# Performance work log

Measured on AMD Instinct MI355X. Metric: run time of the kernel, lower is better.

## Reference

```python
import jax, jax.numpy as jnp
import numpy as np

BS, DIM, N_CLASSES = 4096, 512, 100
POS_W, NEG_W = 2.0, 40.0
MARGIN, POS_T, NEG_T = 0.1, 0.5, 0.5


def setup_inputs() -> dict:
    key = jax.random.key(0)
    k1, k2 = jax.random.split(key)
    x = jax.random.normal(k1, (BS, DIM), dtype=jnp.float32)
    x = x / jnp.linalg.norm(x, axis=-1, keepdims=True)  # cosine-mode embeddings
    labels = jax.random.randint(k2, (BS,), 0, N_CLASSES, dtype=jnp.int64 if jax.config.jax_enable_x64 else jnp.int32)
    return {"batch": x, "labels": labels}


def _masked_logsumexp(sims, mask, use_max):
    # Faithful port of Criterion.masked_logsumexp with dim=0 (per-column).
    m = sims * mask  # bool mask promotes; masked-out entries become 0
    ref = jnp.max(m, axis=0) if use_max else jnp.min(m, axis=0)  # (BS,)
    ref = jax.lax.stop_gradient(ref)
    nz = (jnp.max(m, axis=0) + jnp.min(m, axis=0)) != 0  # columns with any nonzero masked entry
    s = jnp.sum(jnp.exp(sims - ref[None, :]) * mask, axis=0)  # (BS,)
    vals = jnp.log(jnp.where(nz, s, 1.0)) + ref
    return vals, nz


def _masked_mean_softplus(vals, nz, w):
    cnt = jnp.sum(nz).astype(vals.dtype)
    sp = jax.nn.softplus(vals) / w
    mean = jnp.sum(jnp.where(nz, sp, 0.0)) / jnp.maximum(cnt, 1.0)
    # torch path returns scalar 0 from masked_logsumexp when no nz columns -> softplus(0)/w
    return jnp.where(cnt > 0, mean, jax.nn.softplus(0.0) / w)


def reference(batch, labels):
    sim = batch @ batch.T                                  # (BS, BS) cosine similarity
    same = labels[:, None] == labels[None, :]
    diff = ~same
    eye = jnp.eye(sim.shape[0], dtype=bool)

    # per-row bounds: hardest positive (min sim, excl. self) / hardest negative (max sim)
    pos_bound = jnp.min(jnp.where(same & ~eye, sim, jnp.inf), axis=1)   # (BS,)
    neg_bound = jnp.max(jnp.where(diff, sim, -jnp.inf), axis=1)        # (BS,)

    # torch broadcasting applies bounds per-COLUMN (last dim)
    neg_mask = diff & (sim + MARGIN > pos_bound[None, :])
    pos_mask = same & (sim - MARGIN < neg_bound[None, :])

    w_pos = -POS_W * (sim - POS_T)
    w_neg = NEG_W * (sim - NEG_T)

    pos_vals, pos_nz = _masked_logsumexp(w_pos, pos_mask, use_max=False)
    neg_vals, neg_nz = _masked_logsumexp(w_neg, neg_mask, use_max=True)

    loss = _masked_mean_softplus(pos_vals, pos_nz, POS_W) \
         + _masked_mean_softplus(neg_vals, neg_nz, NEG_W)
    return loss
```

## Files before the change

kernel.cpp:

```cpp
#include <hip/hip_runtime.h>
#include <stdint.h>


#define BS 4096
#define DIM 512
#define NTILES 528
#define NSLOT 32

typedef __attribute__((ext_vector_type(8))) short short8;
typedef __attribute__((ext_vector_type(4))) float f32x4;

#define TILE_USH (128 * 64)

__device__ __forceinline__ ushort f2bf(float f){
  unsigned u = __float_as_uint(f);
  return (ushort)((u + 0x7fffu + ((u >> 16) & 1u)) >> 16);
}
__device__ __forceinline__ void gld_lds16(void* ldsp, const void* gp){
  __builtin_amdgcn_global_load_lds((const __attribute__((address_space(1))) void*)gp,
                                   (__attribute__((address_space(3))) void*)ldsp, 16, 0, 0);
}

__global__ void k_convert(const float* __restrict__ x, ushort* __restrict__ xh){
  int i = blockIdx.x * blockDim.x + threadIdx.x;
  float4 v = ((const float4*)x)[i];
  ((ushort4*)xh)[i] = make_ushort4(f2bf(v.x), f2bf(v.y), f2bf(v.z), f2bf(v.w));
}

__device__ __forceinline__ void decode_tile(int bid, int& Rm, int& Rn, bool& diag){
  int wg = (bid & 7) * 66 + (bid >> 3);
  int ii = wg, bm = 0;
  while (ii >= 32 - bm){ ii -= 32 - bm; ++bm; }
  const int bn = bm + ii;
  diag = (bm == bn);
  Rm = bm * 128; Rn = bn * 128;
}

__device__ __forceinline__ void gemm_tile(f32x4 (&acc)[4][4], ushort* lds,
                                          const ushort* __restrict__ Xh,
                                          int Rm, int Rn, int t)
{
  const int l  = t & 63;
  const int w  = t >> 6;
  const int wm = w >> 1, wn = w & 1;
  const int lc = l & 15;
  const int lq = l >> 4;
  const int r0 = t >> 3;
  const int gx = (t & 7) ^ (r0 & 7);
  const int lds_i = t * 8;

  #pragma unroll
  for (int i = 0; i < 4; ++i)
    #pragma unroll
    for (int j = 0; j < 4; ++j) acc[i][j] = (f32x4){0.f, 0.f, 0.f, 0.f};

  for (int ks = 0; ks < 8; ++ks){
    const int kb = ks * 64 + gx * 8;
    #pragma unroll
    for (int rep = 0; rep < 4; ++rep){
      const int row = rep * 32 + r0;
      const int lo  = rep * 2048 + lds_i;
      gld_lds16(&lds[lo],            Xh + (size_t)(Rm + row) * DIM + kb);
      gld_lds16(&lds[TILE_USH + lo], Xh + (size_t)(Rn + row) * DIM + kb);
    }
    __syncthreads();
    #pragma unroll
    for (int kk = 0; kk < 2; ++kk){
      const int gr = kk * 4 + lq;
      const int sl = (gr ^ (l & 7)) * 8;
      short8 ah[4], bh[4];
      #pragma unroll
      for (int f = 0; f < 4; ++f){
        ah[f] = *(const short8*)&lds[(wm * 64 + f * 16 + lc) * 64 + sl];
        bh[f] = *(const short8*)&lds[TILE_USH + (wn * 64 + f * 16 + lc) * 64 + sl];
      }
      #pragma unroll
      for (int fm = 0; fm < 4; ++fm)
        #pragma unroll
        for (int fn = 0; fn < 4; ++fn)
          acc[fm][fn] = __builtin_amdgcn_mfma_f32_16x16x32_bf16(ah[fm], bh[fn], acc[fm][fn], 0, 0, 0);
    }
    __syncthreads();
  }
}

__global__ __launch_bounds__(256)
void k_bounds(const ushort* __restrict__ Xh, const int* __restrict__ labels,
              float* __restrict__ posB, float* __restrict__ negB)
{
  __shared__ ushort lds[2 * TILE_USH];
  const int t = threadIdx.x;
  int Rm, Rn; bool diag;
  decode_tile((int)blockIdx.x, Rm, Rn, diag);
  const int bm = Rm >> 7, bn = Rn >> 7;

  f32x4 acc[4][4];
  gemm_tile(acc, lds, Xh, Rm, Rn, t);

  const int l  = t & 63;
  const int w  = t >> 6;
  const int wm = w >> 1, wn = w & 1;
  const int lc = l & 15, lq = l >> 4;
  const float INF = __builtin_inff();

  int labr[4][4];
  #pragma unroll
  for (int fm = 0; fm < 4; ++fm)
    #pragma unroll
    for (int v = 0; v < 4; ++v)
      labr[fm][v] = labels[Rm + wm * 64 + fm * 16 + lq * 4 + v];

  float* sMnS = (float*)lds;
  float* sMxS = sMnS + 256;
  float* sMnT = sMnS + 512;
  float* sMxT = sMnS + 768;

  #pragma unroll
  for (int fm = 0; fm < 4; ++fm){
    float mn[4] = {INF, INF, INF, INF};
    float mx[4] = {-INF, -INF, -INF, -INF};
    #pragma unroll
    for (int fn = 0; fn < 4; ++fn){
      const int gc = Rn + wn * 64 + fn * 16 + lc;
      const int labc = labels[gc];
      #pragma unroll
      for (int v = 0; v < 4; ++v){
        const float s = acc[fm][fn][v];
        const int grow = Rm + wm * 64 + fm * 16 + lq * 4 + v;
        const bool same = (labc == labr[fm][v]);
        mn[v] = fminf(mn[v], (same && (grow != gc)) ? s : INF);
        mx[v] = fmaxf(mx[v], same ? -INF : s);
      }
    }
    #pragma unroll
    for (int off = 1; off < 16; off <<= 1)
      #pragma unroll
      for (int v = 0; v < 4; ++v){
        mn[v] = fminf(mn[v], __shfl_xor(mn[v], off));
        mx[v] = fmaxf(mx[v], __shfl_xor(mx[v], off));
      }
    if (lc == 0){
      #pragma unroll
      for (int v = 0; v < 4; ++v){
        const int r64 = fm * 16 + lq * 4 + v;
        sMnS[(wm * 2 + wn) * 64 + r64] = mn[v];
        sMxS[(wm * 2 + wn) * 64 + r64] = mx[v];
      }
    }
  }
  if (!diag){
    #pragma unroll
    for (int fn = 0; fn < 4; ++fn){
      const int gc = Rn + wn * 64 + fn * 16 + lc;
      const int labc = labels[gc];
      float mn = INF, mx = -INF;
      #pragma unroll
      for (int fm = 0; fm < 4; ++fm)
        #pragma unroll
        for (int v = 0; v < 4; ++v){
          const float s = acc[fm][fn][v];
          const bool same = (labc == labr[fm][v]);
          mn = fminf(mn, same ? s : INF);
          mx = fmaxf(mx, same ? -INF : s);
        }
      #pragma unroll
      for (int off = 16; off < 64; off <<= 1){
        mn = fminf(mn, __shfl_xor(mn, off));
        mx = fmaxf(mx, __shfl_xor(mx, off));
      }
      if (l < 16){
        const int c64 = fn * 16 + lc;
        sMnT[(wn * 2 + wm) * 64 + c64] = mn;
        sMxT[(wn * 2 + wm) * 64 + c64] = mx;
      }
    }
  }
  __syncthreads();
  if (t < 128){
    const int h = t >> 6, r = t & 63;
    posB[(size_t)bn * BS + Rm + t] = fminf(sMnS[(h * 2 + 0) * 64 + r], sMnS[(h * 2 + 1) * 64 + r]);
    negB[(size_t)bn * BS + Rm + t] = fmaxf(sMxS[(h * 2 + 0) * 64 + r], sMxS[(h * 2 + 1) * 64 + r]);
    if (!diag){
      posB[(size_t)bm * BS + Rn + t] = fminf(sMnT[(h * 2 + 0) * 64 + r], sMnT[(h * 2 + 1) * 64 + r]);
      negB[(size_t)bm * BS + Rn + t] = fmaxf(sMxT[(h * 2 + 0) * 64 + r], sMxT[(h * 2 + 1) * 64 + r]);
    }
  }
}

__global__ void k_redbounds(const float* __restrict__ posB, const float* __restrict__ negB,
                            float* __restrict__ pos_bound, float* __restrict__ neg_bound){
  const int r = blockIdx.x * 256 + threadIdx.x;
  float mn = __builtin_inff(), mx = -__builtin_inff();
  #pragma unroll
  for (int s = 0; s < NSLOT; ++s){
    mn = fminf(mn, posB[(size_t)s * BS + r]);
    mx = fmaxf(mx, negB[(size_t)s * BS + r]);
  }
  pos_bound[r] = mn;
  neg_bound[r] = mx;
}

__global__ __launch_bounds__(256)
void k_stats(const ushort* __restrict__ Xh, const int* __restrict__ labels,
             const float* __restrict__ pos_bound, const float* __restrict__ neg_bound,
             float* __restrict__ SNp, float* __restrict__ SPp)
{
  __shared__ ushort lds[2 * TILE_USH];
  const int t = threadIdx.x;
  int Rm, Rn; bool diag;
  decode_tile((int)blockIdx.x, Rm, Rn, diag);
  const int bm = Rm >> 7, bn = Rn >> 7;

  f32x4 acc[4][4];
  gemm_tile(acc, lds, Xh, Rm, Rn, t);

  const int l  = t & 63;
  const int w  = t >> 6;
  const int wm = w >> 1, wn = w & 1;
  const int lc = l & 15, lq = l >> 4;

  int labr[4][4];
  #pragma unroll
  for (int fm = 0; fm < 4; ++fm)
    #pragma unroll
    for (int v = 0; v < 4; ++v)
      labr[fm][v] = labels[Rm + wm * 64 + fm * 16 + lq * 4 + v];

  float* sSNs = (float*)lds;
  float* sSPs = sSNs + 256;
  float* sSNt = sSNs + 512;
  float* sSPt = sSNs + 768;

  #pragma unroll
  for (int fn = 0; fn < 4; ++fn){
    const int gc = Rn + wn * 64 + fn * 16 + lc;
    const int labc = labels[gc];
    const float pb = pos_bound[gc];
    const float nb = neg_bound[gc];
    float sN = 0.f, sP = 0.f;
    #pragma unroll
    for (int fm = 0; fm < 4; ++fm)
      #pragma unroll
      for (int v = 0; v < 4; ++v){
        const float s = acc[fm][fn][v];
        const bool same = (labc == labr[fm][v]);
        sN += ((!same) && (s + 0.1f > pb)) ? __expf(40.0f * (s - 0.5f)) : 0.0f;
        sP += (same && (s - 0.1f < nb))    ? __expf(-2.0f * (s - 0.5f)) : 0.0f;
      }
    #pragma unroll
    for (int off = 16; off < 64; off <<= 1){
      sN += __shfl_xor(sN, off);
      sP += __shfl_xor(sP, off);
    }
    if (l < 16){
      const int c64 = fn * 16 + lc;
      sSNs[(wn * 2 + wm) * 64 + c64] = sN;
      sSPs[(wn * 2 + wm) * 64 + c64] = sP;
    }
  }
  if (!diag){
    #pragma unroll
    for (int fm = 0; fm < 4; ++fm){
      float pbr[4], nbr[4];
      #pragma unroll
      for (int v = 0; v < 4; ++v){
        const int grow = Rm + wm * 64 + fm * 16 + lq * 4 + v;
        pbr[v] = pos_bound[grow];
        nbr[v] = neg_bound[grow];
      }
      float sN[4] = {0.f, 0.f, 0.f, 0.f}, sP[4] = {0.f, 0.f, 0.f, 0.f};
      #pragma unroll
      for (int fn = 0; fn < 4; ++fn){
        const int gc = Rn + wn * 64 + fn * 16 + lc;
        const int labc = labels[gc];
        #pragma unroll
        for (int v = 0; v < 4; ++v){
          const float s = acc[fm][fn][v];
          const bool same = (labc == labr[fm][v]);
          sN[v] += ((!same) && (s + 0.1f > pbr[v])) ? __expf(40.0f * (s - 0.5f)) : 0.0f;
          sP[v] += (same && (s - 0.1f < nbr[v]))    ? __expf(-2.0f * (s - 0.5f)) : 0.0f;
        }
      }
      #pragma unroll
      for (int off = 1; off < 16; off <<= 1)
        #pragma unroll
        for (int v = 0; v < 4; ++v){
          sN[v] += __shfl_xor(sN[v], off);
          sP[v] += __shfl_xor(sP[v], off);
        }
      if (lc == 0){
        #pragma unroll
        for (int v = 0; v < 4; ++v){
          const int r64 = fm * 16 + lq * 4 + v;
          sSNt[(wm * 2 + wn) * 64 + r64] = sN[v];
          sSPt[(wm * 2 + wn) * 64 + r64] = sP[v];
        }
      }
    }
  }
  __syncthreads();
  if (t < 128){
    const int h = t >> 6, r = t & 63;
    SNp[(size_t)bm * BS + Rn + t] = sSNs[(h * 2 + 0) * 64 + r] + sSNs[(h * 2 + 1) * 64 + r];
    SPp[(size_t)bm * BS + Rn + t] = sSPs[(h * 2 + 0) * 64 + r] + sSPs[(h * 2 + 1) * 64 + r];
    if (!diag){
      SNp[(size_t)bn * BS + Rm + t] = sSNt[(h * 2 + 0) * 64 + r] + sSNt[(h * 2 + 1) * 64 + r];
      SPp[(size_t)bn * BS + Rm + t] = sSPt[(h * 2 + 0) * 64 + r] + sSPt[(h * 2 + 1) * 64 + r];
    }
  }
}

__global__ void k_finalize(const float* __restrict__ SNp, const float* __restrict__ SPp,
                           float* __restrict__ out)
{
  const int t = threadIdx.x;
  float sumP = 0.f, cP = 0.f, sumN = 0.f, cN = 0.f;
  #pragma unroll
  for (int i = 0; i < 4; ++i){
    const int c = t + i * 1024;
    float sn = 0.f, sp = 0.f;
    #pragma unroll
    for (int s = 0; s < NSLOT; ++s){
      sn += SNp[(size_t)s * BS + c];
      sp += SPp[(size_t)s * BS + c];
    }
    if (sn != 0.0f){ sumN += log1pf(sn); cN += 1.0f; }
    if (sp != 0.0f){ sumP += log1pf(sp); cP += 1.0f; }
  }
  #pragma unroll
  for (int off = 32; off; off >>= 1){
    sumP += __shfl_down(sumP, off); cP += __shfl_down(cP, off);
    sumN += __shfl_down(sumN, off); cN += __shfl_down(cN, off);
  }
  __shared__ float red[16][4];
  const int w = t >> 6;
  if ((t & 63) == 0){ red[w][0] = sumP; red[w][1] = cP; red[w][2] = sumN; red[w][3] = cN; }
  __syncthreads();
  if (t == 0){
    float SPs = 0.f, CPs = 0.f, SNs = 0.f, CNs = 0.f;
    for (int i = 0; i < 16; ++i){ SPs += red[i][0]; CPs += red[i][1]; SNs += red[i][2]; CNs += red[i][3]; }
    const float LN2 = 0.69314718055994531f;
    const float tP = (CPs > 0.f) ? (SPs / 2.0f)  / fmaxf(CPs, 1.f) : LN2 / 2.0f;
    const float tN = (CNs > 0.f) ? (SNs / 40.0f) / fmaxf(CNs, 1.f) : LN2 / 40.0f;
    out[0] = tP + tN;
  }
}

extern "C" void kernel_launch(void* const* d_in, const int* in_sizes, int n_in,
                              void* d_out, int out_size, void* d_ws, size_t ws_size,
                              hipStream_t stream) {
  const float* x    = (const float*)d_in[0];
  const int* labels = (const int*)d_in[1];
  char* W = (char*)d_ws;
  ushort* Xh        = (ushort*)W;
  float*  P1        = (float*)(W + (4u << 20));
  float*  P2        = (float*)(W + (4u << 20) + (512u << 10));
  float*  pos_bound = (float*)(W + (5u << 20));
  float*  neg_bound = (float*)(W + (5u << 20) + (16u << 10));

  k_convert<<<(BS * DIM / 4) / 256, 256, 0, stream>>>(x, Xh);
  k_bounds<<<NTILES, 256, 0, stream>>>(Xh, labels, P1, P2);
  k_redbounds<<<BS / 256, 256, 0, stream>>>(P1, P2, pos_bound, neg_bound);
  k_stats<<<NTILES, 256, 0, stream>>>(Xh, labels, pos_bound, neg_bound, P1, P2);
  k_finalize<<<1, 1024, 0, stream>>>(P1, P2, (float*)d_out);
}
```

Before: 179.4 us.

## Double-buffer GEMM K-slices in LDS and parallelize final stats reduction

The shared GEMM tile loop now double-buffers its LDS staging. It issues the global-to-LDS loads for the next K-slice before running MFMAs on the current one, which hides memory latency behind compute, and the per-iteration syncs become explicit vmcnt waits plus barriers. The single-block finalize kernel is split into a 16-block column reduction that writes partials, followed by a tiny final kernel. This spreads the tail reduction across CUs at the cost of one extra launch. LDS use per block doubles to 64 KB, which may reduce occupancy.

```diff
diff --git a/kernel.cpp b/kernel.cpp
--- a/kernel.cpp
+++ b/kernel.cpp
@@ -11,6 +11,8 @@
 typedef __attribute__((ext_vector_type(4))) float f32x4;
 
 #define TILE_USH (128 * 64)
+
+#define VMW0 asm volatile("s_waitcnt vmcnt(0)" ::: "memory")
 
 __device__ __forceinline__ ushort f2bf(float f){
   unsigned u = __float_as_uint(f);
@@ -36,9 +38,24 @@
   Rm = bm * 128; Rn = bn * 128;
 }
 
-__device__ __forceinline__ void gemm_tile(f32x4 (&acc)[4][4], ushort* lds,
-                                          const ushort* __restrict__ Xh,
-                                          int Rm, int Rn, int t)
+__device__ __forceinline__ void stage_ks(ushort* dstA, ushort* dstB,
+                                         const ushort* __restrict__ Xh,
+                                         int Rm, int Rn, int ks,
+                                         int r0, int gx, int lds_i){
+  const int kb = ks * 64 + gx * 8;
+  #pragma unroll
+  for (int rep = 0; rep < 4; ++rep){
+    const int row = rep * 32 + r0;
+    const int lo  = rep * 2048 + lds_i;
+    gld_lds16(dstA + lo, Xh + (size_t)(Rm + row) * DIM + kb);
+    gld_lds16(dstB + lo, Xh + (size_t)(Rn + row) * DIM + kb);
+  }
+}
+
+__device__ __forceinline__ void gemm_tile_db(f32x4 (&acc)[4][4],
+                                             ushort (&lds)[2][2 * TILE_USH],
+                                             const ushort* __restrict__ Xh,
+                                             int Rm, int Rn, int t)
 {
   const int l  = t & 63;
   const int w  = t >> 6;
@@ -54,16 +71,16 @@
     #pragma unroll
     for (int j = 0; j < 4; ++j) acc[i][j] = (f32x4){0.f, 0.f, 0.f, 0.f};
 
+  stage_ks(&lds[0][0], &lds[0][TILE_USH], Xh, Rm, Rn, 0, r0, gx, lds_i);
+  VMW0;
+  __builtin_amdgcn_s_barrier();
+  __builtin_amdgcn_sched_barrier(0);
+
+  #pragma unroll
   for (int ks = 0; ks < 8; ++ks){
-    const int kb = ks * 64 + gx * 8;
-    #pragma unroll
-    for (int rep = 0; rep < 4; ++rep){
-      const int row = rep * 32 + r0;
-      const int lo  = rep * 2048 + lds_i;
-      gld_lds16(&lds[lo],            Xh + (size_t)(Rm + row) * DIM + kb);
-      gld_lds16(&lds[TILE_USH + lo], Xh + (size_t)(Rn + row) * DIM + kb);
-    }
-    __syncthreads();
+    const int cur = ks & 1;
+    if (ks < 7)
+      stage_ks(&lds[cur ^ 1][0], &lds[cur ^ 1][TILE_USH], Xh, Rm, Rn, ks + 1, r0, gx, lds_i);
     #pragma unroll
     for (int kk = 0; kk < 2; ++kk){
       const int gr = kk * 4 + lq;
@@ -71,8 +88,8 @@
       short8 ah[4], bh[4];
       #pragma unroll
       for (int f = 0; f < 4; ++f){
-        ah[f] = *(const short8*)&lds[(wm * 64 + f * 16 + lc) * 64 + sl];
-        bh[f] = *(const short8*)&lds[TILE_USH + (wn * 64 + f * 16 + lc) * 64 + sl];
+        ah[f] = *(const short8*)&lds[cur][(wm * 64 + f * 16 + lc) * 64 + sl];
+        bh[f] = *(const short8*)&lds[cur][TILE_USH + (wn * 64 + f * 16 + lc) * 64 + sl];
       }
       #pragma unroll
       for (int fm = 0; fm < 4; ++fm)
@@ -80,7 +97,10 @@
         for (int fn = 0; fn < 4; ++fn)
           acc[fm][fn] = __builtin_amdgcn_mfma_f32_16x16x32_bf16(ah[fm], bh[fn], acc[fm][fn], 0, 0, 0);
     }
-    __syncthreads();
+    __builtin_amdgcn_sched_barrier(0);
+    VMW0;
+    __builtin_amdgcn_s_barrier();
+    __builtin_amdgcn_sched_barrier(0);
   }
 }
 
@@ -88,14 +108,14 @@
 void k_bounds(const ushort* __restrict__ Xh, const int* __restrict__ labels,
               float* __restrict__ posB, float* __restrict__ negB)
 {
-  __shared__ ushort lds[2 * TILE_USH];
+  __shared__ ushort lds[2][2 * TILE_USH];
   const int t = threadIdx.x;
   int Rm, Rn; bool diag;
   decode_tile((int)blockIdx.x, Rm, Rn, diag);
   const int bm = Rm >> 7, bn = Rn >> 7;
 
   f32x4 acc[4][4];
-  gemm_tile(acc, lds, Xh, Rm, Rn, t);
+  gemm_tile_db(acc, lds, Xh, Rm, Rn, t);
 
   const int l  = t & 63;
   const int w  = t >> 6;
@@ -110,7 +130,8 @@
     for (int v = 0; v < 4; ++v)
       labr[fm][v] = labels[Rm + wm * 64 + fm * 16 + lq * 4 + v];
 
-  float* sMnS = (float*)lds;
+  __syncthreads();
+  float* sMnS = (float*)&lds[0][0];
   float* sMxS = sMnS + 256;
   float* sMnT = sMnS + 512;
   float* sMxT = sMnS + 768;
@@ -205,14 +226,14 @@
              const float* __restrict__ pos_bound, const float* __restrict__ neg_bound,
              float* __restrict__ SNp, float* __restrict__ SPp)
 {
-  __shared__ ushort lds[2 * TILE_USH];
+  __shared__ ushort lds[2][2 * TILE_USH];
   const int t = threadIdx.x;
   int Rm, Rn; bool diag;
   decode_tile((int)blockIdx.x, Rm, Rn, diag);
   const int bm = Rm >> 7, bn = Rn >> 7;
 
   f32x4 acc[4][4];
-  gemm_tile(acc, lds, Xh, Rm, Rn, t);
+  gemm_tile_db(acc, lds, Xh, Rm, Rn, t);
 
   const int l  = t & 63;
   const int w  = t >> 6;
@@ -226,7 +247,8 @@
     for (int v = 0; v < 4; ++v)
       labr[fm][v] = labels[Rm + wm * 64 + fm * 16 + lq * 4 + v];
 
-  float* sSNs = (float*)lds;
+  __syncthreads();
+  float* sSNs = (float*)&lds[0][0];
   float* sSPs = sSNs + 256;
   float* sSNt = sSNs + 512;
   float* sSPt = sSNs + 768;
@@ -310,38 +332,51 @@
   }
 }
 
-__global__ void k_finalize(const float* __restrict__ SNp, const float* __restrict__ SPp,
-                           float* __restrict__ out)
+__global__ void k_redstats(const float* __restrict__ SNp, const float* __restrict__ SPp,
+                           float4* __restrict__ part)
 {
   const int t = threadIdx.x;
-  float sumP = 0.f, cP = 0.f, sumN = 0.f, cN = 0.f;
-  #pragma unroll
-  for (int i = 0; i < 4; ++i){
-    const int c = t + i * 1024;
-    float sn = 0.f, sp = 0.f;
-    #pragma unroll
-    for (int s = 0; s < NSLOT; ++s){
-      sn += SNp[(size_t)s * BS + c];
-      sp += SPp[(size_t)s * BS + c];
-    }
-    if (sn != 0.0f){ sumN += log1pf(sn); cN += 1.0f; }
-    if (sp != 0.0f){ sumP += log1pf(sp); cP += 1.0f; }
-  }
+  const int c = blockIdx.x * 256 + t;
+  float sn = 0.f, sp = 0.f;
+  #pragma unroll
+  for (int s = 0; s < NSLOT; ++s){
+    sn += SNp[(size_t)s * BS + c];
+    sp += SPp[(size_t)s * BS + c];
+  }
+  float sumP = (sp != 0.f) ? log1pf(sp) : 0.f;
+  float cP   = (sp != 0.f) ? 1.f : 0.f;
+  float sumN = (sn != 0.f) ? log1pf(sn) : 0.f;
+  float cN   = (sn != 0.f) ? 1.f : 0.f;
   #pragma unroll
   for (int off = 32; off; off >>= 1){
     sumP += __shfl_down(sumP, off); cP += __shfl_down(cP, off);
     sumN += __shfl_down(sumN, off); cN += __shfl_down(cN, off);
   }
-  __shared__ float red[16][4];
+  __shared__ float red[4][4];
   const int w = t >> 6;
   if ((t & 63) == 0){ red[w][0] = sumP; red[w][1] = cP; red[w][2] = sumN; red[w][3] = cN; }
   __syncthreads();
   if (t == 0){
-    float SPs = 0.f, CPs = 0.f, SNs = 0.f, CNs = 0.f;
-    for (int i = 0; i < 16; ++i){ SPs += red[i][0]; CPs += red[i][1]; SNs += red[i][2]; CNs += red[i][3]; }
+    float a = 0.f, b = 0.f, c2 = 0.f, d = 0.f;
+    for (int i = 0; i < 4; ++i){ a += red[i][0]; b += red[i][1]; c2 += red[i][2]; d += red[i][3]; }
+    part[blockIdx.x] = make_float4(a, b, c2, d);
+  }
+}
+
+__global__ void k_final2(const float4* __restrict__ part, float* __restrict__ out)
+{
+  const int l = threadIdx.x;
+  float4 v = (l < 16) ? part[l] : make_float4(0.f, 0.f, 0.f, 0.f);
+  float sumP = v.x, cP = v.y, sumN = v.z, cN = v.w;
+  #pragma unroll
+  for (int off = 8; off; off >>= 1){
+    sumP += __shfl_down(sumP, off); cP += __shfl_down(cP, off);
+    sumN += __shfl_down(sumN, off); cN += __shfl_down(cN, off);
+  }
+  if (l == 0){
     const float LN2 = 0.69314718055994531f;
-    const float tP = (CPs > 0.f) ? (SPs / 2.0f)  / fmaxf(CPs, 1.f) : LN2 / 2.0f;
-    const float tN = (CNs > 0.f) ? (SNs / 40.0f) / fmaxf(CNs, 1.f) : LN2 / 40.0f;
+    const float tP = (cP > 0.f) ? (sumP / 2.0f)  / fmaxf(cP, 1.f) : LN2 / 2.0f;
+    const float tN = (cN > 0.f) ? (sumN / 40.0f) / fmaxf(cN, 1.f) : LN2 / 40.0f;
     out[0] = tP + tN;
   }
 }
@@ -357,10 +392,12 @@
   float*  P2        = (float*)(W + (4u << 20) + (512u << 10));
   float*  pos_bound = (float*)(W + (5u << 20));
   float*  neg_bound = (float*)(W + (5u << 20) + (16u << 10));
+  float4* part      = (float4*)(W + (5u << 20) + (32u << 10));
 
   k_convert<<<(BS * DIM / 4) / 256, 256, 0, stream>>>(x, Xh);
   k_bounds<<<NTILES, 256, 0, stream>>>(Xh, labels, P1, P2);
   k_redbounds<<<BS / 256, 256, 0, stream>>>(P1, P2, pos_bound, neg_bound);
   k_stats<<<NTILES, 256, 0, stream>>>(Xh, labels, pos_bound, neg_bound, P1, P2);
-  k_finalize<<<1, 1024, 0, stream>>>(P1, P2, (float*)d_out);
-}
+  k_redstats<<<BS / 256, 256, 0, stream>>>(P1, P2, part);
+  k_final2<<<1, 64, 0, stream>>>(part, (float*)d_out);
+}
```

Measured after the change: 151.6 us. -15.5%, faster.
